# Kernel optimization log

Measured on AMD Instinct MI355X. Metric: run time of the kernel, lower is better.

Reference implementation:

```python
import jax, jax.numpy as jnp
import numpy as np

N = 100000       # nodes
E = 1600000      # edges (avg degree 16)
D_IN = 128
D_HID = 32
D_OUT = 32
H = 4            # heads
NEG_SLOPE = 0.2  # GATConv default leaky_relu slope


def setup_inputs() -> dict:
    key = jax.random.key(0)
    ks = jax.random.split(key, 10)
    s = 0.1
    return {
        "edge": jax.random.randint(ks[0], (2, E), 0, N),
        "features": jax.random.normal(ks[1], (N, D_IN), jnp.float32),
        # layer 1 params: W [in, H*hid], attention vectors per head [H, hid]
        "W1": jax.random.normal(ks[2], (D_IN, H * D_HID), jnp.float32) * s,
        "a1_src": jax.random.normal(ks[3], (H, D_HID), jnp.float32) * s,
        "a1_dst": jax.random.normal(ks[4], (H, D_HID), jnp.float32) * s,
        "b1": jnp.zeros((H * D_HID,), jnp.float32),
        # layer 2 params
        "W2": jax.random.normal(ks[5], (H * D_HID, H * D_OUT), jnp.float32) * s,
        "a2_src": jax.random.normal(ks[6], (H, D_OUT), jnp.float32) * s,
        "a2_dst": jax.random.normal(ks[7], (H, D_OUT), jnp.float32) * s,
        "b2": jnp.zeros((H * D_OUT,), jnp.float32),
    }


def gat_conv(x, src, dst, W, a_src, a_dst, b, heads, d_out):
    """Multi-head GAT layer, concat heads. x: [N, d_in] -> [N, heads*d_out]."""
    n = x.shape[0]
    h = (x @ W).reshape(n, heads, d_out)                 # [N,H,D]
    e_src = jnp.einsum('nhd,hd->nh', h, a_src)           # [N,H]
    e_dst = jnp.einsum('nhd,hd->nh', h, a_dst)           # [N,H]
    e = jax.nn.leaky_relu(e_src[src] + e_dst[dst], NEG_SLOPE)  # [E,H]
    # softmax over incoming edges of each dst node (stable via segment max)
    m = jax.lax.stop_gradient(jax.ops.segment_max(e, dst, num_segments=n))
    w = jnp.exp(e - m[dst])                              # [E,H]
    den = jax.ops.segment_sum(w, dst, num_segments=n)    # [N,H]
    alpha = w / den[dst]                                 # [E,H]
    out = jax.ops.segment_sum(alpha[:, :, None] * h[src], dst, num_segments=n)
    return out.reshape(n, heads * d_out) + b


def reference(edge, features, W1, a1_src, a1_dst, b1, W2, a2_src, a2_dst, b2):
    src, dst = edge[0], edge[1]
    h = jax.nn.relu(gat_conv(features, src, dst, W1, a1_src, a1_dst, b1, H, D_HID))
    h = gat_conv(h, src, dst, W2, a2_src, a2_dst, b2, H, D_OUT)
    return jax.nn.log_softmax(h, axis=1)
```

## Files before the change

kernel.cpp:

```cpp
#include <hip/hip_runtime.h>
#include <hip/hip_bf16.h>
#include <math.h>

#define N_NODES 100000
#define N_EDGES 1600000
#define NHEADS 4
#define NEG_SLOPE 0.2f
#define NB 1563
#define KSUB 8
#define SUBCAP 224
#define BCAPT (KSUB * SUBCAP)
#define CPAD 32

typedef __attribute__((ext_vector_type(8))) short short8;
typedef __attribute__((ext_vector_type(4))) float f32x4;
typedef __attribute__((ext_vector_type(2))) float f32x2;

__device__ __forceinline__ unsigned short f2bf(float f) {
    unsigned int u = __float_as_uint(f);
    u += 0x7fffu + ((u >> 16) & 1u);
    return (unsigned short)(u >> 16);
}
__device__ __forceinline__ f32x2 bfpair(unsigned int u) {
    f32x2 r;
    r.x = __uint_as_float(u << 16);
    r.y = __uint_as_float(u & 0xffff0000u);
    return r;
}
__device__ __forceinline__ short8 pack8(float4 f0, float4 f1) {
    short8 v;
    v[0] = (short)f2bf(f0.x); v[1] = (short)f2bf(f0.y);
    v[2] = (short)f2bf(f0.z); v[3] = (short)f2bf(f0.w);
    v[4] = (short)f2bf(f1.x); v[5] = (short)f2bf(f1.y);
    v[6] = (short)f2bf(f1.z); v[7] = (short)f2bf(f1.w);
    return v;
}

__global__ void pack_w_kernel(const float* __restrict__ W,
                              const float* __restrict__ a_src,
                              const float* __restrict__ a_dst,
                              unsigned short* __restrict__ Wp) {
    int idx = blockIdx.x * 256 + threadIdx.x;
    if (idx >= 18432) return;
    int j    = idx & 7;
    int lane = (idx >> 3) & 63;
    int kc   = (idx >> 9) & 3;
    int ct   = idx >> 11;
    int k = kc * 32 + ((lane >> 4) & 3) * 8 + j;
    int n = lane & 15;
    float v = 0.f;
    if (ct < 8) {
        v = W[k * 128 + ct * 16 + n];
    } else if (n < 8) {
        int hd = n & 3;
        const float* av = (n < 4 ? a_src : a_dst) + hd * 32;
        const float* wr = W + k * 128 + hd * 32;
#pragma unroll
        for (int t = 0; t < 32; ++t) v = fmaf(wr[t], av[t], v);
    }
    Wp[idx] = f2bf(v);
}

template <bool XF32>
__global__ __launch_bounds__(256) void gemm_mfma_kernel(
        const void* __restrict__ xv,
        const unsigned short* __restrict__ Wp,
        unsigned short* __restrict__ h, float* __restrict__ esd, int n_rows) {
    __shared__ unsigned short Wl[18432];

    const int t = threadIdx.x;
    {
        const uint4* s4 = (const uint4*)Wp;
        uint4* d4 = (uint4*)Wl;
#pragma unroll
        for (int p = 0; p < 9; ++p) d4[p * 256 + t] = s4[p * 256 + t];
    }
    __syncthreads();

    const int lane = t & 63, wave = t >> 6;
    const int l15 = lane & 15, quad = lane >> 4;
    const int rbase = blockIdx.x * 128 + wave * 32;

    short8 a[2][4];
#pragma unroll
    for (int rt = 0; rt < 2; ++rt) {
        int r = rbase + rt * 16 + l15;
        r = r < n_rows ? r : n_rows - 1;
        if (XF32) {
            const float* xr = (const float*)xv + (size_t)r * 128 + quad * 8;
#pragma unroll
            for (int kc = 0; kc < 4; ++kc) {
                float4 f0 = *(const float4*)(xr + kc * 32);
                float4 f1 = *(const float4*)(xr + kc * 32 + 4);
                a[rt][kc] = pack8(f0, f1);
            }
        } else {
            const unsigned short* xr =
                (const unsigned short*)xv + (size_t)r * 128 + quad * 8;
#pragma unroll
            for (int kc = 0; kc < 4; ++kc)
                a[rt][kc] = *(const short8*)(xr + kc * 32);
        }
    }

    f32x4 acc[2][9];
#pragma unroll
    for (int rt = 0; rt < 2; ++rt)
#pragma unroll
        for (int ct = 0; ct < 9; ++ct)
            acc[rt][ct] = (f32x4){0.f, 0.f, 0.f, 0.f};

#pragma unroll
    for (int ct = 0; ct < 9; ++ct) {
#pragma unroll
        for (int kc = 0; kc < 4; ++kc) {
            short8 b = *(const short8*)&Wl[((ct * 4 + kc) * 64 + lane) * 8];
            acc[0][ct] = __builtin_amdgcn_mfma_f32_16x16x32_bf16(
                a[0][kc], b, acc[0][ct], 0, 0, 0);
            acc[1][ct] = __builtin_amdgcn_mfma_f32_16x16x32_bf16(
                a[1][kc], b, acc[1][ct], 0, 0, 0);
        }
    }

#pragma unroll
    for (int rt = 0; rt < 2; ++rt) {
#pragma unroll
        for (int i = 0; i < 4; ++i) {
            int r = rbase + rt * 16 + quad * 4 + i;
            if (r < n_rows) {
                unsigned short* hp = h + (size_t)r * 128 + l15;
#pragma unroll
                for (int ct = 0; ct < 8; ++ct)
                    hp[ct * 16] = f2bf(acc[rt][ct][i]);
                if (l15 < 8) esd[r * 8 + l15] = acc[rt][8][i];
            }
        }
    }
}

__global__ void zero_ints_kernel(int* __restrict__ p, int n) {
    int i = blockIdx.x * 256 + threadIdx.x;
    if (i < n) p[i] = 0;
}

__global__ void bucket_fill_kernel(const int* __restrict__ src,
                                   const int* __restrict__ dst,
                                   int* __restrict__ bcnt,
                                   unsigned int* __restrict__ slab) {
    int e = blockIdx.x * 256 + threadIdx.x;
    if (e >= N_EDGES) return;
    int d = __builtin_nontemporal_load(dst + e);
    int s = __builtin_nontemporal_load(src + e);
    int b = d >> 6;
    int sub = blockIdx.x & (KSUB - 1);
    int c = b * KSUB + sub;
    int pos = atomicAdd(&bcnt[c * CPAD], 1);
    slab[(size_t)b * BCAPT + sub * SUBCAP + pos] =
        (unsigned int)s | ((unsigned int)(d & 63) << 17);
}

__global__ __launch_bounds__(1024) void bucket_scan_kernel(
        const int* __restrict__ bcnt, int* __restrict__ bbase,
        int* __restrict__ rowptr) {
    __shared__ int ws[16];
    const int t = threadIdx.x;
    const int lane = t & 63, wave = t >> 6;
    if (t == 0) rowptr[N_NODES] = N_EDGES;
    int carry = 0;
#pragma unroll
    for (int pass = 0; pass < 2; ++pass) {
        int b = pass * 1024 + t;
        int tot = 0;
        if (b < NB) {
#pragma unroll
            for (int s = 0; s < KSUB; ++s) tot += bcnt[(b * KSUB + s) * CPAD];
        }
        int v = tot;
#pragma unroll
        for (int off = 1; off < 64; off <<= 1) {
            int u = __shfl_up(v, off);
            if (lane >= off) v += u;
        }
        if (lane == 63) ws[wave] = v;
        __syncthreads();
        int woff = 0, btot = 0;
#pragma unroll
        for (int w = 0; w < 16; ++w) {
            if (w < wave) woff += ws[w];
            btot += ws[w];
        }
        if (b < NB) bbase[b] = carry + woff + v - tot;
        carry += btot;
        __syncthreads();
    }
}

__global__ __launch_bounds__(256) void bucket_build_kernel(
        const int* __restrict__ bcnt, const unsigned int* __restrict__ slab,
        const int* __restrict__ bbase, int* __restrict__ rowptr,
        int* __restrict__ csr_src) {
    __shared__ int hist[64];
    __shared__ int rp[64];
    __shared__ int cnt[64];
    const int b = blockIdx.x;
    const int t = threadIdx.x;
    if (t < 64) { hist[t] = 0; cnt[t] = 0; }
    __syncthreads();
    const int lane = t & 63, wave = t >> 6;
    const unsigned int* sp = slab + (size_t)b * BCAPT;
#pragma unroll
    for (int s = wave; s < KSUB; s += 4) {
        const int m = bcnt[(b * KSUB + s) * CPAD];
        for (int i = lane; i < m; i += 64)
            atomicAdd(&hist[sp[s * SUBCAP + i] >> 17], 1);
    }
    __syncthreads();
    if (wave == 0) {
        int h = hist[lane];
        int v = h;
#pragma unroll
        for (int off = 1; off < 64; off <<= 1) {
            int u = __shfl_up(v, off);
            if (lane >= off) v += u;
        }
        int r = bbase[b] + v - h;
        rp[lane] = r;
        int node = b * 64 + lane;
        if (node < N_NODES) rowptr[node] = r;
    }
    __syncthreads();
#pragma unroll
    for (int s = wave; s < KSUB; s += 4) {
        const int m = bcnt[(b * KSUB + s) * CPAD];
        for (int i = lane; i < m; i += 64) {
            unsigned int rec = sp[s * SUBCAP + i];
            int local = rec >> 17;
            int pos = rp[local] + atomicAdd(&cnt[local], 1);
            csr_src[pos] = (int)(rec & 0x1FFFFu);
        }
    }
}

template <bool LOGSOFTMAX>
__global__ __launch_bounds__(256) void aggregate_kernel(
        const int* __restrict__ csr_src, const int* __restrict__ rowptr,
        const float* __restrict__ esd,
        const unsigned short* __restrict__ hb, const float* __restrict__ b,
        void* __restrict__ out) {
    const int lane = threadIdx.x & 63;
    const int wave = threadIdx.x >> 6;
    const int n = blockIdx.x * 4 + wave;
    if (n >= N_NODES) return;
    const int eo = lane >> 4;
    const int cl = lane & 15;
    const int c0 = cl * 8;
    const int hd = cl >> 2;
    const float edn = esd[n * 8 + 4 + hd];
    const int base = rowptr[n];
    const int dg = rowptr[n + 1] - base;

    f32x2 acc2[4];
#pragma unroll
    for (int j = 0; j < 4; ++j) acc2[j] = (f32x2){0.f, 0.f};
    float wsum = 0.f;

    if (dg > 0) {
        const int myidx = csr_src[base + (lane < dg ? lane : dg - 1)];
        const int nit = (dg + 3) >> 2;
        const unsigned hbo = (unsigned)c0 * 2u;
        const unsigned edo = (unsigned)hd * 4u;
        const char* hbp = (const char*)hb;
        const char* esp = (const char*)esd;

        auto getS = [&](int j) -> int {
            int o = 4 * j + eo;
            if (4 * j < 64) return __shfl(myidx, o);
            int oc = o < dg ? o : dg - 1;
            return csr_src[base + oc];
        };
        auto loadP = [&](int s) -> uint4 {
            return *(const uint4*)(hbp + (((unsigned)s << 8) + hbo));
        };
        auto loadE = [&](int s, int j) -> float {
            float e = *(const float*)(esp + (((unsigned)s << 5) + edo));
            return (4 * j + eo < dg) ? e : -1e30f;
        };

        int s0 = getS(0);
        uint4 p0 = loadP(s0);
        float e0 = loadE(s0, 0);
        uint4 p1 = p0; float e1 = e0;
        if (nit > 1) {
            int s1 = getS(1);
            p1 = loadP(s1);
            e1 = loadE(s1, 1);
        }
#pragma unroll 2
        for (int j = 0; j < nit; ++j) {
            uint4 p2 = p1; float e2 = e1;
            if (j + 2 < nit) {
                int s2 = getS(j + 2);
                p2 = loadP(s2);
                e2 = loadE(s2, j + 2);
            }
            float sc = e0 + edn;
            sc = sc > 0.f ? sc : NEG_SLOPE * sc;
            float w = __expf(sc);
            f32x2 wv = {w, w};
            acc2[0] = __builtin_elementwise_fma(wv, bfpair(p0.x), acc2[0]);
            acc2[1] = __builtin_elementwise_fma(wv, bfpair(p0.y), acc2[1]);
            acc2[2] = __builtin_elementwise_fma(wv, bfpair(p0.z), acc2[2]);
            acc2[3] = __builtin_elementwise_fma(wv, bfpair(p0.w), acc2[3]);
            wsum += w;
            p0 = p1; e0 = e1; p1 = p2; e1 = e2;
        }
    }

    float acc[8];
#pragma unroll
    for (int j = 0; j < 4; ++j) {
        acc[2 * j]     = acc2[j].x;
        acc[2 * j + 1] = acc2[j].y;
    }

#pragma unroll
    for (int j = 0; j < 8; ++j) {
        acc[j] += __shfl_xor(acc[j], 16);
        acc[j] += __shfl_xor(acc[j], 32);
    }
    wsum += __shfl_xor(wsum, 16);
    wsum += __shfl_xor(wsum, 32);

    float inv = wsum > 0.f ? 1.f / wsum : 0.f;
    float bl[8];
    *(float4*)&bl[0] = *(const float4*)(b + c0);
    *(float4*)&bl[4] = *(const float4*)(b + c0 + 4);
    float v[8];
#pragma unroll
    for (int j = 0; j < 8; ++j) v[j] = acc[j] * inv + bl[j];

    if (!LOGSOFTMAX) {
        if (lane < 16) {
            unsigned int pk[4];
#pragma unroll
            for (int j = 0; j < 4; ++j) {
                float r0 = v[2 * j]     > 0.f ? v[2 * j]     : 0.f;
                float r1 = v[2 * j + 1] > 0.f ? v[2 * j + 1] : 0.f;
                pk[j] = (unsigned int)f2bf(r0) | ((unsigned int)f2bf(r1) << 16);
            }
            *(uint4*)((unsigned short*)out + (size_t)n * 128 + c0) =
                make_uint4(pk[0], pk[1], pk[2], pk[3]);
        }
    } else {
        float m = v[0];
#pragma unroll
        for (int j = 1; j < 8; ++j) m = fmaxf(m, v[j]);
#pragma unroll
        for (int s = 1; s < 16; s <<= 1) m = fmaxf(m, __shfl_xor(m, s));
        float se = 0.f;
#pragma unroll
        for (int j = 0; j < 8; ++j) se += __expf(v[j] - m);
#pragma unroll
        for (int s = 1; s < 16; s <<= 1) se += __shfl_xor(se, s);
        float ls = m + logf(se);
        if (lane < 16) {
            float* o = (float*)out + (size_t)n * 128 + c0;
            *(float4*)o = make_float4(v[0] - ls, v[1] - ls, v[2] - ls, v[3] - ls);
            *(float4*)(o + 4) = make_float4(v[4] - ls, v[5] - ls, v[6] - ls, v[7] - ls);
        }
    }
}

extern "C" void kernel_launch(void* const* d_in, const int* in_sizes, int n_in,
                              void* d_out, int out_size, void* d_ws, size_t ws_size,
                              hipStream_t stream) {
    const int*   edge = (const int*)d_in[0];
    const int*   src  = edge;
    const int*   dst  = edge + N_EDGES;
    const float* feat = (const float*)d_in[1];
    const float* W1   = (const float*)d_in[2];
    const float* a1s  = (const float*)d_in[3];
    const float* a1d  = (const float*)d_in[4];
    const float* b1   = (const float*)d_in[5];
    const float* W2   = (const float*)d_in[6];
    const float* a2s  = (const float*)d_in[7];
    const float* a2d  = (const float*)d_in[8];
    const float* b2   = (const float*)d_in[9];
    float* out = (float*)d_out;

    unsigned short* hb  = (unsigned short*)d_ws;
    unsigned short* x1b = hb + (size_t)N_NODES * 128;
    unsigned short* Wp1 = x1b + (size_t)N_NODES * 128;
    unsigned short* Wp2 = Wp1 + 18432;
    float* esd = (float*)(Wp2 + 18432);
    int* rowptr   = (int*)(esd + (size_t)N_NODES * 8);
    int* bbase    = rowptr + (N_NODES + 1);
    int* bcnt     = bbase + NB;
    unsigned int* slab = (unsigned int*)(bcnt + NB * KSUB * CPAD);
    int* csr_src  = (int*)(slab + (size_t)NB * BCAPT);

    const int edge_blk  = (N_EDGES + 255) / 256;
    const int gemm_blk  = (N_NODES + 127) / 128;
    const int agg_blk   = (N_NODES + 3) / 4;
    const int nctr      = NB * KSUB * CPAD;

    zero_ints_kernel<<<(nctr + 255) / 256, 256, 0, stream>>>(bcnt, nctr);
    bucket_fill_kernel<<<edge_blk, 256, 0, stream>>>(src, dst, bcnt, slab);
    bucket_scan_kernel<<<1, 1024, 0, stream>>>(bcnt, bbase, rowptr);
    bucket_build_kernel<<<NB, 256, 0, stream>>>(bcnt, slab, bbase, rowptr, csr_src);

    pack_w_kernel<<<72, 256, 0, stream>>>(W1, a1s, a1d, Wp1);
    pack_w_kernel<<<72, 256, 0, stream>>>(W2, a2s, a2d, Wp2);

    gemm_mfma_kernel<true><<<gemm_blk, 256, 0, stream>>>(feat, Wp1, hb, esd, N_NODES);
    aggregate_kernel<false><<<agg_blk, 256, 0, stream>>>(
        csr_src, rowptr, esd, hb, b1, x1b);

    gemm_mfma_kernel<false><<<gemm_blk, 256, 0, stream>>>(x1b, Wp2, hb, esd, N_NODES);
    aggregate_kernel<true><<<agg_blk, 256, 0, stream>>>(
        csr_src, rowptr, esd, hb, b2, out);
}
```

Measured before the change: 399.9 us.

## Replace global-atomic bucket CSR build with two-pass counting radix scatter

```diff
diff --git a/kernel.cpp b/kernel.cpp
--- a/kernel.cpp
+++ b/kernel.cpp
@@ -6,11 +6,12 @@
 #define N_EDGES 1600000
 #define NHEADS 4
 #define NEG_SLOPE 0.2f
-#define NB 1563
-#define KSUB 8
-#define SUBCAP 224
-#define BCAPT (KSUB * SUBCAP)
-#define CPAD 32
+#define NSUP 49
+#define CHUNK 4096
+#define NBLK ((N_EDGES + CHUNK - 1) / CHUNK)
+#define NGC (NSUP * NBLK)
+#define SUBB 2048
+#define LCAP 128
 
 typedef __attribute__((ext_vector_type(8))) short short8;
 typedef __attribute__((ext_vector_type(4))) float f32x4;
@@ -138,44 +139,34 @@
     }
 }
 
-__global__ void zero_ints_kernel(int* __restrict__ p, int n) {
-    int i = blockIdx.x * 256 + threadIdx.x;
-    if (i < n) p[i] = 0;
-}
-
-__global__ void bucket_fill_kernel(const int* __restrict__ src,
-                                   const int* __restrict__ dst,
-                                   int* __restrict__ bcnt,
-                                   unsigned int* __restrict__ slab) {
-    int e = blockIdx.x * 256 + threadIdx.x;
-    if (e >= N_EDGES) return;
-    int d = __builtin_nontemporal_load(dst + e);
-    int s = __builtin_nontemporal_load(src + e);
-    int b = d >> 6;
-    int sub = blockIdx.x & (KSUB - 1);
-    int c = b * KSUB + sub;
-    int pos = atomicAdd(&bcnt[c * CPAD], 1);
-    slab[(size_t)b * BCAPT + sub * SUBCAP + pos] =
-        (unsigned int)s | ((unsigned int)(d & 63) << 17);
-}
-
-__global__ __launch_bounds__(1024) void bucket_scan_kernel(
-        const int* __restrict__ bcnt, int* __restrict__ bbase,
+
+__global__ __launch_bounds__(256) void count_kernel(
+        const int* __restrict__ dst, int* __restrict__ gcnt) {
+    __shared__ int hist[NSUP];
+    const int t = threadIdx.x;
+    if (t < NSUP) hist[t] = 0;
+    __syncthreads();
+    const int e0 = blockIdx.x * CHUNK;
+#pragma unroll
+    for (int k = 0; k < CHUNK / 256; ++k) {
+        int e = e0 + k * 256 + t;
+        if (e < N_EDGES) atomicAdd(&hist[dst[e] >> 11], 1);
+    }
+    __syncthreads();
+    if (t < NSUP) gcnt[t * NBLK + blockIdx.x] = hist[t];
+}
+
+__global__ __launch_bounds__(1024) void offset_scan_kernel(
+        int* __restrict__ gcnt, int* __restrict__ sbase,
         int* __restrict__ rowptr) {
     __shared__ int ws[16];
-    const int t = threadIdx.x;
-    const int lane = t & 63, wave = t >> 6;
-    if (t == 0) rowptr[N_NODES] = N_EDGES;
+    const int t = threadIdx.x, lane = t & 63, wave = t >> 6;
     int carry = 0;
-#pragma unroll
-    for (int pass = 0; pass < 2; ++pass) {
-        int b = pass * 1024 + t;
-        int tot = 0;
-        if (b < NB) {
-#pragma unroll
-            for (int s = 0; s < KSUB; ++s) tot += bcnt[(b * KSUB + s) * CPAD];
-        }
-        int v = tot;
+    const int npass = (NGC + 1023) / 1024;
+    for (int p = 0; p < npass; ++p) {
+        int idx = p * 1024 + t;
+        int val = (idx < NGC) ? gcnt[idx] : 0;
+        int v = val;
 #pragma unroll
         for (int off = 1; off < 64; off <<= 1) {
             int u = __shfl_up(v, off);
@@ -183,61 +174,98 @@
         }
         if (lane == 63) ws[wave] = v;
         __syncthreads();
-        int woff = 0, btot = 0;
-#pragma unroll
-        for (int w = 0; w < 16; ++w) {
-            if (w < wave) woff += ws[w];
-            btot += ws[w];
-        }
-        if (b < NB) bbase[b] = carry + woff + v - tot;
-        carry += btot;
-        __syncthreads();
-    }
-}
-
-__global__ __launch_bounds__(256) void bucket_build_kernel(
-        const int* __restrict__ bcnt, const unsigned int* __restrict__ slab,
-        const int* __restrict__ bbase, int* __restrict__ rowptr,
-        int* __restrict__ csr_src) {
-    __shared__ int hist[64];
-    __shared__ int rp[64];
-    __shared__ int cnt[64];
+        int woff = 0, tot = 0;
+#pragma unroll
+        for (int w = 0; w < 16; ++w) { if (w < wave) woff += ws[w]; tot += ws[w]; }
+        if (idx < NGC) gcnt[idx] = carry + woff + v - val;
+        carry += tot;
+        __syncthreads();
+    }
+    if (t < NSUP) sbase[t] = gcnt[t * NBLK];
+    if (t == 0) { sbase[NSUP] = N_EDGES; rowptr[N_NODES] = N_EDGES; }
+}
+
+__global__ __launch_bounds__(256) void scatter_kernel(
+        const int* __restrict__ src, const int* __restrict__ dst,
+        const int* __restrict__ gcnt, unsigned int* __restrict__ sslab) {
+    __shared__ unsigned int lists[NSUP * LCAP];
+    __shared__ int lcnt[NSUP];
+    __shared__ int written[NSUP];
+    const int t = threadIdx.x;
     const int b = blockIdx.x;
-    const int t = threadIdx.x;
-    if (t < 64) { hist[t] = 0; cnt[t] = 0; }
-    __syncthreads();
-    const int lane = t & 63, wave = t >> 6;
-    const unsigned int* sp = slab + (size_t)b * BCAPT;
-#pragma unroll
-    for (int s = wave; s < KSUB; s += 4) {
-        const int m = bcnt[(b * KSUB + s) * CPAD];
-        for (int i = lane; i < m; i += 64)
-            atomicAdd(&hist[sp[s * SUBCAP + i] >> 17], 1);
-    }
-    __syncthreads();
-    if (wave == 0) {
-        int h = hist[lane];
-        int v = h;
-#pragma unroll
-        for (int off = 1; off < 64; off <<= 1) {
-            int u = __shfl_up(v, off);
-            if (lane >= off) v += u;
-        }
-        int r = bbase[b] + v - h;
-        rp[lane] = r;
-        int node = b * 64 + lane;
-        if (node < N_NODES) rowptr[node] = r;
-    }
-    __syncthreads();
-#pragma unroll
-    for (int s = wave; s < KSUB; s += 4) {
-        const int m = bcnt[(b * KSUB + s) * CPAD];
-        for (int i = lane; i < m; i += 64) {
-            unsigned int rec = sp[s * SUBCAP + i];
-            int local = rec >> 17;
-            int pos = rp[local] + atomicAdd(&cnt[local], 1);
-            csr_src[pos] = (int)(rec & 0x1FFFFu);
-        }
+    if (t < NSUP) written[t] = 0;
+    const int e0 = b * CHUNK;
+    for (int sb = 0; sb < CHUNK / SUBB; ++sb) {
+        if (t < NSUP) lcnt[t] = 0;
+        __syncthreads();
+#pragma unroll
+        for (int k = 0; k < SUBB / 256; ++k) {
+            int e = e0 + sb * SUBB + k * 256 + t;
+            if (e < N_EDGES) {
+                int d = dst[e];
+                int s = d >> 11;
+                int pos = atomicAdd(&lcnt[s], 1);
+                if (pos < LCAP)
+                    lists[s * LCAP + pos] =
+                        (unsigned)src[e] | ((unsigned)(d & 2047) << 17);
+            }
+        }
+        __syncthreads();
+        for (int s = 0; s < NSUP; ++s) {
+            int n = lcnt[s]; n = n > LCAP ? LCAP : n;
+            int base = gcnt[s * NBLK + b] + written[s];
+            for (int i = t; i < n; i += 256)
+                sslab[base + i] = lists[s * LCAP + i];
+        }
+        __syncthreads();
+        if (t < NSUP) {
+            int n = lcnt[t]; n = n > LCAP ? LCAP : n;
+            written[t] += n;
+        }
+        __syncthreads();
+    }
+}
+
+__global__ __launch_bounds__(1024) void super_build_kernel(
+        const unsigned int* __restrict__ sslab, const int* __restrict__ sbase,
+        int* __restrict__ rowptr, int* __restrict__ csr_src) {
+    __shared__ int hist[2048];
+    __shared__ int ws[16];
+    const int s = blockIdx.x;
+    const int t = threadIdx.x, lane = t & 63, wave = t >> 6;
+    const int lo = sbase[s], hi = sbase[s + 1];
+    hist[t] = 0; hist[t + 1024] = 0;
+    __syncthreads();
+    for (int i = lo + t; i < hi; i += 1024)
+        atomicAdd(&hist[sslab[i] >> 17], 1);
+    __syncthreads();
+    int a = hist[2 * t], bq = hist[2 * t + 1];
+    int sum = a + bq;
+    int v = sum;
+#pragma unroll
+    for (int off = 1; off < 64; off <<= 1) {
+        int u = __shfl_up(v, off);
+        if (lane >= off) v += u;
+    }
+    if (lane == 63) ws[wave] = v;
+    __syncthreads();
+    int woff = 0;
+#pragma unroll
+    for (int w = 0; w < 16; ++w) if (w < wave) woff += ws[w];
+    int excl = woff + v - sum;
+    __syncthreads();
+    hist[2 * t] = excl;
+    hist[2 * t + 1] = excl + a;
+    __syncthreads();
+    const int node0 = s * 2048;
+    if (node0 + 2 * t < N_NODES)     rowptr[node0 + 2 * t]     = lo + hist[2 * t];
+    if (node0 + 2 * t + 1 < N_NODES) rowptr[node0 + 2 * t + 1] = lo + hist[2 * t + 1];
+    __syncthreads();
+    for (int i = lo + t; i < hi; i += 1024) {
+        unsigned int rec = sslab[i];
+        int loc = rec >> 17;
+        int pos = lo + atomicAdd(&hist[loc], 1);
+        csr_src[pos] = (int)(rec & 0x1FFFFu);
     }
 }
 
@@ -394,20 +422,18 @@
     unsigned short* Wp2 = Wp1 + 18432;
     float* esd = (float*)(Wp2 + 18432);
     int* rowptr   = (int*)(esd + (size_t)N_NODES * 8);
-    int* bbase    = rowptr + (N_NODES + 1);
-    int* bcnt     = bbase + NB;
-    unsigned int* slab = (unsigned int*)(bcnt + NB * KSUB * CPAD);
-    int* csr_src  = (int*)(slab + (size_t)NB * BCAPT);
-
-    const int edge_blk  = (N_EDGES + 255) / 256;
+    int* sbase    = rowptr + (N_NODES + 1);
+    int* gcnt     = sbase + (NSUP + 1);
+    unsigned int* sslab = (unsigned int*)(gcnt + NGC);
+    int* csr_src  = (int*)(sslab + (size_t)N_EDGES);
+
     const int gemm_blk  = (N_NODES + 127) / 128;
     const int agg_blk   = (N_NODES + 3) / 4;
-    const int nctr      = NB * KSUB * CPAD;
-
-    zero_ints_kernel<<<(nctr + 255) / 256, 256, 0, stream>>>(bcnt, nctr);
-    bucket_fill_kernel<<<edge_blk, 256, 0, stream>>>(src, dst, bcnt, slab);
-    bucket_scan_kernel<<<1, 1024, 0, stream>>>(bcnt, bbase, rowptr);
-    bucket_build_kernel<<<NB, 256, 0, stream>>>(bcnt, slab, bbase, rowptr, csr_src);
+
+    count_kernel<<<NBLK, 256, 0, stream>>>(dst, gcnt);
+    offset_scan_kernel<<<1, 1024, 0, stream>>>(gcnt, sbase, rowptr);
+    scatter_kernel<<<NBLK, 256, 0, stream>>>(src, dst, gcnt, sslab);
+    super_build_kernel<<<NSUP, 1024, 0, stream>>>(sslab, sbase, rowptr, csr_src);
 
     pack_w_kernel<<<72, 256, 0, stream>>>(W1, a1s, a1d, Wp1);
     pack_w_kernel<<<72, 256, 0, stream>>>(W2, a2s, a2d, Wp2);
```

New measurement: 388.2 us. 2.9% less time.
